# Optimization experiments

Measured on AMD Instinct MI355X. Metric: run time of the kernel, lower is better.

## Reference

```python
import jax, jax.numpy as jnp
import numpy as np


def _dilate(x, ker):
    """Grayscale (max-plus) dilation, TF tf.nn.dilation2d semantics, SAME pad, stride 1.

    x:   [B,H,W,C] or [B,H,W,C,F]
    ker: [kh,kw,C,F]
    out: [B,H,W,C,F] = max_{dy,dx} x_pad[b, h+dy, w+dx, c(,f)] + ker[dy,dx,c,f]
    """
    kh, kw = ker.shape[0], ker.shape[1]
    pt, pl = (kh - 1) // 2, (kw - 1) // 2
    pb, pr = kh - 1 - pt, kw - 1 - pl
    if x.ndim == 4:
        x = x[..., None]  # broadcast over filter axis
    B, H, W = x.shape[0], x.shape[1], x.shape[2]
    xp = jnp.pad(x, ((0, 0), (pt, pb), (pl, pr), (0, 0), (0, 0)),
                 constant_values=-jnp.inf)
    out = None
    for dy in range(kh):
        for dx in range(kw):
            v = xp[:, dy:dy + H, dx:dx + W] + ker[dy, dx]  # [B,H,W,C,F]
            out = v if out is None else jnp.maximum(out, v)
    return out


def _erode(x, ker):
    # TF identity: erosion2d(v, f) = -dilation2d(-v, spatially-flipped f)
    return -_dilate(-x, ker[::-1, ::-1])


def _opening_p4(x, kernel):
    # x: [B,4,H,W,C], kernel: [kh,kw,3,C,F]
    kero = jnp.stack([jnp.rot90(kernel[:, :, 2], 3, axes=(0, 1)),
                      kernel[:, :, 1],
                      jnp.rot90(kernel[:, :, 0], 1, axes=(0, 1))], axis=2)
    y = jnp.concatenate([x[:, -1:], x, x[:, :1]], axis=1)  # wrap group axis -> [B,6,H,W,C]
    ero = []
    for j in range(4):
        kr = jnp.rot90(kero, j, axes=(0, 1))  # [kh,kw,3,C,F]
        d = jnp.stack([_erode(y[:, j + k], kr[:, :, k]) for k in range(3)], axis=-1)
        ero.append(jnp.min(d, axis=-1))  # min over SE depth -> [B,H,W,C,F]
    ero = jnp.stack(ero, axis=1)  # [B,4,H,W,C,F]
    ep = jnp.concatenate([ero[:, -1:], ero, ero[:, :1]], axis=1)  # [B,6,H,W,C,F]
    outs = []
    for j in range(4):
        kr = jnp.rot90(kernel, j, axes=(0, 1))
        d = jnp.stack([_dilate(ep[:, j + k], kr[:, :, k]) for k in range(3)], axis=-1)
        outs.append(jnp.max(d, axis=-1))  # max over SE depth -> [B,H,W,C,F]
    open_res = jnp.stack(outs, axis=1)  # [B,4,H,W,C,F]
    return jnp.sum(open_res, axis=-2)   # sum over input channels -> [B,4,H,W,F]


def setup_inputs() -> dict:
    key = jax.random.key(0)
    k1, k2 = jax.random.split(key)
    x = jax.random.normal(k1, (4, 4, 64, 64, 8), dtype=jnp.float32)
    kernel = jax.random.normal(k2, (3, 3, 3, 8, 16), dtype=jnp.float32) * 0.1
    return {"x": x, "kernel": kernel}


def reference(x, kernel):
    return _opening_p4(x, kernel)
```

## Files before the change

kernel.cpp:

```cpp
#include <hip/hip_runtime.h>


#define HH 64
#define WW 64
#define NEG_INF (-__builtin_inff())
#define POS_INF (__builtin_inff())

#define ROT_G(G, A, B, I, J) do { switch (G) { \
    case 0:  I = (A);     J = (B);     break; \
    case 1:  I = (B);     J = 2 - (A); break; \
    case 2:  I = 2 - (A); J = 2 - (B); break; \
    default: I = 2 - (B); J = (A);     break; } } while (0)

typedef _Float16 hv4 __attribute__((ext_vector_type(4)));

__device__ __forceinline__ hv4 f4_to_hv4(float4 v) {
    hv4 r;
    r.x = (_Float16)v.x; r.y = (_Float16)v.y;
    r.z = (_Float16)v.z; r.w = (_Float16)v.w;
    return r;
}

__global__ __launch_bounds__(256) void erode_t(const float* __restrict__ x,
                                               const float* __restrict__ ker,
                                               hv4* __restrict__ ero) {
    __shared__ __align__(16) float xs[9 * 8 * 68];

    const int tid = threadIdx.x;
    const int h = blockIdx.x & 63;
    const int g = (blockIdx.x >> 6) & 3;
    const int b = blockIdx.x >> 8;

    const float4* x4 = (const float4*)x;
    const float4* ker4 = (const float4*)ker;

    for (int t = tid; t < 1188; t += 256) {
        int q01 = t & 1;
        int u = t >> 1;
        int wp = u % 66;
        int v = u / 66;
        int r = v % 3;
        int p = v / 3;
        int g2 = (g + p + 3) & 3;
        int h2 = h - 1 + r;
        int w2 = wp - 1;
        float4 vv;
        if ((unsigned)h2 < HH && (unsigned)w2 < WW)
            vv = x4[(((b * 4 + g2) * HH + h2) * WW + w2) * 2 + q01];
        else
            vv = make_float4(POS_INF, POS_INF, POS_INF, POS_INF);
        int rowb = (p * 3 + r) * 8 + q01 * 4;
        xs[(rowb + 0) * 68 + wp] = vv.x;
        xs[(rowb + 1) * 68 + wp] = vv.y;
        xs[(rowb + 2) * 68 + wp] = vv.z;
        xs[(rowb + 3) * 68 + wp] = vv.w;
    }
    __syncthreads();

    const int q = tid & 3;
    const int c = (tid >> 2) & 7;
    const int slot = tid >> 5;
    const float4* xs4 = (const float4*)xs;

    float4 acc[8];
#pragma unroll
    for (int i = 0; i < 8; ++i)
        acc[i] = make_float4(POS_INF, POS_INF, POS_INF, POS_INF);

#pragma unroll
    for (int k2 = 0; k2 < 3; ++k2) {
        float4 ke9[9];
#pragma unroll
        for (int t9 = 0; t9 < 9; ++t9) {
            int dy = t9 / 3, dx = t9 % 3;
            int a0 = 2 - dy, b0 = 2 - dx;
            int i, jj;
            ROT_G(g, a0, b0, i, jj);
            int ka, kb, kc;
            if (k2 == 0)      { ka = 2 - jj; kb = i;      kc = 2; }
            else if (k2 == 1) { ka = i;      kb = jj;     kc = 1; }
            else              { ka = jj;     kb = 2 - i;  kc = 0; }
            ke9[t9] = ker4[((ka * 3 + kb) * 3 + kc) * 32 + c * 4 + q];
        }
#pragma unroll
        for (int dy = 0; dy < 3; ++dy) {
            const int base4 = ((k2 * 3 + dy) * 8 + c) * 17 + slot * 2;
            float4 xa = xs4[base4];
            float4 xb = xs4[base4 + 1];
            float4 xc = xs4[base4 + 2];
            float xw[12] = {xa.x, xa.y, xa.z, xa.w,
                            xb.x, xb.y, xb.z, xb.w,
                            xc.x, xc.y, xc.z, xc.w};
#pragma unroll
            for (int dx = 0; dx < 3; ++dx) {
                float4 kv = ke9[dy * 3 + dx];
#pragma unroll
                for (int i = 0; i < 8; ++i) {
                    float v = xw[i + dx];
                    acc[i].x = fminf(acc[i].x, v - kv.x);
                    acc[i].y = fminf(acc[i].y, v - kv.y);
                    acc[i].z = fminf(acc[i].z, v - kv.z);
                    acc[i].w = fminf(acc[i].w, v - kv.w);
                }
            }
        }
    }

    const int row = (b * 4 + g) * HH + h;
    const size_t obase = ((size_t)row * 66 + slot * 8 + 1) * 32 + c * 4 + q;
#pragma unroll
    for (int i = 0; i < 8; ++i)
        ero[obase + (size_t)i * 32] = f4_to_hv4(acc[i]);

    const hv4 ninf = {(_Float16)NEG_INF, (_Float16)NEG_INF,
                      (_Float16)NEG_INF, (_Float16)NEG_INF};
    if (tid < 32)
        ero[(size_t)row * 66 * 32 + tid] = ninf;
    else if (tid < 64)
        ero[((size_t)row * 66 + 65) * 32 + (tid - 32)] = ninf;
}

__global__ __launch_bounds__(256) void dilate_t(const hv4* __restrict__ ero,
                                                const float* __restrict__ ker,
                                                float* __restrict__ out) {
    const int tid = threadIdx.x;
    const int q = tid & 3;
    const int c = (tid >> 2) & 7;
    const int slot = tid >> 5;
    const int ws = blockIdx.x & 7;
    const int hs = (blockIdx.x >> 3) & 7;
    const int j = (blockIdx.x >> 6) & 3;
    const int b = blockIdx.x >> 8;
    const int w = ws * 8 + slot;

    const float4* ker4 = (const float4*)ker;

    const hv4 ninf = {(_Float16)NEG_INF, (_Float16)NEG_INF,
                      (_Float16)NEG_INF, (_Float16)NEG_INF};
    hv4 acc[8];
#pragma unroll
    for (int r = 0; r < 8; ++r)
        acc[r] = ninf;

#pragma unroll
    for (int k = 0; k < 3; ++k) {
        const int gsrc = (j + k + 3) & 3;
        hv4 kd9[9];
#pragma unroll
        for (int t9 = 0; t9 < 9; ++t9) {
            int dy = t9 / 3, dx = t9 % 3;
            int i, jj;
            ROT_G(j, dy, dx, i, jj);
            kd9[t9] = f4_to_hv4(ker4[((i * 3 + jj) * 3 + k) * 32 + c * 4 + q]);
        }
        const size_t pb = ((size_t)(b * 4 + gsrc) * HH * 66 + w) * 32 + c * 4 + q;
#pragma unroll
        for (int ei = 0; ei < 10; ++ei) {
            const int er = hs * 8 - 1 + ei;
            if ((unsigned)er >= HH) continue;
            const size_t rb = pb + (size_t)er * 66 * 32;
            hv4 e0 = ero[rb];
            hv4 e1 = ero[rb + 32];
            hv4 e2 = ero[rb + 64];
#pragma unroll
            for (int dy = 0; dy < 3; ++dy) {
                const int rr = ei - dy;
                if ((unsigned)rr >= 8) continue;
                acc[rr] = __builtin_elementwise_max(acc[rr], e0 + kd9[dy * 3 + 0]);
                acc[rr] = __builtin_elementwise_max(acc[rr], e1 + kd9[dy * 3 + 1]);
                acc[rr] = __builtin_elementwise_max(acc[rr], e2 + kd9[dy * 3 + 2]);
            }
        }
    }

    float4* out4 = (float4*)out;
    const int bjbase = (b * 4 + j) * HH + hs * 8;
#pragma unroll
    for (int r = 0; r < 8; ++r) {
        float4 s = make_float4((float)acc[r].x, (float)acc[r].y,
                               (float)acc[r].z, (float)acc[r].w);
#pragma unroll
        for (int off = 4; off <= 16; off <<= 1) {
            s.x += __shfl_xor(s.x, off, 64);
            s.y += __shfl_xor(s.y, off, 64);
            s.z += __shfl_xor(s.z, off, 64);
            s.w += __shfl_xor(s.w, off, 64);
        }
        if (c == 0)
            out4[((size_t)(bjbase + r) * WW + w) * 4 + q] = s;
    }
}

__global__ __launch_bounds__(256, 3) void opening_fused_fb(
    const float* __restrict__ x, const float* __restrict__ ker, float* __restrict__ out)
{
    __shared__ __align__(16) float xs[8 * 4 * 144];
    __shared__ float4 es4[4 * 4 * 100];
    __shared__ float4 ke4[27 * 4 * 4];
    __shared__ float4 kd4[9 * 4 * 4];

    const int tid = threadIdx.x;
    const int tileX = blockIdx.x & 7;
    const int tileY = (blockIdx.x >> 3) & 7;
    const int j = (blockIdx.x >> 6) & 3;
    const int b = blockIdx.x >> 8;
    const float4* ker4 = (const float4*)ker;
    const float4* x4 = (const float4*)x;

    for (int t = tid; t < 1152; t += 256) {
        int q01 = t & 1;
        int cell = t >> 1;
        int g = cell / 144;
        int rem = cell - g * 144;
        int r = rem / 12;
        int s = rem - r * 12;
        int h = tileY * 8 - 2 + r;
        int w = tileX * 8 - 2 + s;
        float4 v;
        if ((unsigned)h < HH && (unsigned)w < WW)
            v = x4[(((b * 4 + g) * HH + h) * WW + w) * 2 + q01];
        else
            v = make_float4(POS_INF, POS_INF, POS_INF, POS_INF);
        int c0 = q01 * 4;
        xs[((c0 + 0) * 4 + g) * 144 + rem] = v.x;
        xs[((c0 + 1) * 4 + g) * 144 + rem] = v.y;
        xs[((c0 + 2) * 4 + g) * 144 + rem] = v.z;
        xs[((c0 + 3) * 4 + g) * 144 + rem] = v.w;
    }
    __syncthreads();

    const int q_o = tid & 3;
    const int ox = (tid >> 2) & 7;
    const int oy = tid >> 5;

    float4 acc[8];
#pragma unroll
    for (int c = 0; c < 8; ++c)
        acc[c] = make_float4(NEG_INF, NEG_INF, NEG_INF, NEG_INF);

    for (int k = 0; k < 3; ++k) {
        const int gsrc = (j + k + 3) & 3;
#pragma unroll
        for (int cg = 0; cg < 2; ++cg) {
            for (int t = tid; t < 576; t += 256) {
                if (t < 432) {
                    int q = t & 3;
                    int c4 = (t >> 2) & 3;
                    int tap = t >> 4;
                    int k2 = tap % 3;
                    int dxdy = tap / 3;
                    int dx = dxdy % 3;
                    int dy = dxdy / 3;
                    int a0 = 2 - dy, b0 = 2 - dx;
                    int i, jj;
                    ROT_G(gsrc, a0, b0, i, jj);
                    int ka, kb, kc;
                    if (k2 == 0)      { ka = 2 - jj; kb = i;      kc = 2; }
                    else if (k2 == 1) { ka = i;      kb = jj;     kc = 1; }
                    else              { ka = jj;     kb = 2 - i;  kc = 0; }
                    int c = cg * 4 + c4;
                    ke4[t] = ker4[((ka * 3 + kb) * 3 + kc) * 32 + c * 4 + q];
                } else {
                    int u = t - 432;
                    int q = u & 3;
                    int c4 = (u >> 2) & 3;
                    int dydx = u >> 4;
                    int dx = dydx % 3;
                    int dy = dydx / 3;
                    int i, jj;
                    ROT_G(j, dy, dx, i, jj);
                    int c = cg * 4 + c4;
                    kd4[u] = ker4[((i * 3 + jj) * 3 + k) * 32 + c * 4 + q];
                }
            }
            __syncthreads();

            for (int it = 0; it < 2; ++it) {
                int id = tid + (it << 8);
                int c4 = id >> 7;
                int p = id & 127;
                if (p >= 100) continue;
                int ey = (p * 205) >> 11;
                int ex = p - ey * 10;
                int h_es = tileY * 8 - 1 + ey;
                int w_es = tileX * 8 - 1 + ex;
                float4 b0, b1, b2, b3;
                if ((unsigned)h_es < HH && (unsigned)w_es < WW) {
                    b0 = b1 = b2 = b3 = make_float4(POS_INF, POS_INF, POS_INF, POS_INF);
                    int c = cg * 4 + c4;
#pragma unroll
                    for (int k2 = 0; k2 < 3; ++k2) {
                        int g2 = (gsrc + k2 + 3) & 3;
                        int base = (c * 4 + g2) * 144 + ey * 12 + ex;
#pragma unroll
                        for (int dy = 0; dy < 3; ++dy)
#pragma unroll
                            for (int dx = 0; dx < 3; ++dx) {
                                float v = xs[base + dy * 12 + dx];
                                const float4* kk = &ke4[(((dy * 3 + dx) * 3 + k2) * 4 + c4) * 4];
                                float4 kv;
                                kv = kk[0];
                                b0.x = fminf(b0.x, v - kv.x); b0.y = fminf(b0.y, v - kv.y);
                                b0.z = fminf(b0.z, v - kv.z); b0.w = fminf(b0.w, v - kv.w);
                                kv = kk[1];
                                b1.x = fminf(b1.x, v - kv.x); b1.y = fminf(b1.y, v - kv.y);
                                b1.z = fminf(b1.z, v - kv.z); b1.w = fminf(b1.w, v - kv.w);
                                kv = kk[2];
                                b2.x = fminf(b2.x, v - kv.x); b2.y = fminf(b2.y, v - kv.y);
                                b2.z = fminf(b2.z, v - kv.z); b2.w = fminf(b2.w, v - kv.w);
                                kv = kk[3];
                                b3.x = fminf(b3.x, v - kv.x); b3.y = fminf(b3.y, v - kv.y);
                                b3.z = fminf(b3.z, v - kv.z); b3.w = fminf(b3.w, v - kv.w);
                            }
                    }
                } else {
                    b0 = b1 = b2 = b3 = make_float4(NEG_INF, NEG_INF, NEG_INF, NEG_INF);
                }
                int eb = (c4 * 4) * 100 + p;
                es4[eb] = b0; es4[eb + 100] = b1; es4[eb + 200] = b2; es4[eb + 300] = b3;
            }
            __syncthreads();

#pragma unroll
            for (int c4 = 0; c4 < 4; ++c4) {
                float4 a = acc[cg * 4 + c4];
#pragma unroll
                for (int dy = 0; dy < 3; ++dy)
#pragma unroll
                    for (int dx = 0; dx < 3; ++dx) {
                        int pos = (oy + dy) * 10 + (ox + dx);
                        float4 e = es4[(c4 * 4 + q_o) * 100 + pos];
                        float4 kv = kd4[(dy * 3 + dx) * 16 + c4 * 4 + q_o];
                        a.x = fmaxf(a.x, e.x + kv.x);
                        a.y = fmaxf(a.y, e.y + kv.y);
                        a.z = fmaxf(a.z, e.z + kv.z);
                        a.w = fmaxf(a.w, e.w + kv.w);
                    }
                acc[cg * 4 + c4] = a;
            }
            __syncthreads();
        }
    }

    float4 s = acc[0];
#pragma unroll
    for (int c = 1; c < 8; ++c) {
        s.x += acc[c].x; s.y += acc[c].y; s.z += acc[c].z; s.w += acc[c].w;
    }
    const int h = tileY * 8 + oy;
    const int w = tileX * 8 + ox;
    ((float4*)out)[(((b * 4 + j) * HH + h) * WW + w) * 4 + q_o] = s;
}

extern "C" void kernel_launch(void* const* d_in, const int* in_sizes, int n_in,
                              void* d_out, int out_size, void* d_ws, size_t ws_size,
                              hipStream_t stream) {
    const float* x = (const float*)d_in[0];
    const float* ker = (const float*)d_in[1];
    float* out = (float*)d_out;

    const size_t ero_f16_bytes = (size_t)16 * HH * 66 * 32 * 8;

    if (ws_size >= ero_f16_bytes) {
        hv4* ero = (hv4*)d_ws;
        erode_t<<<1024, 256, 0, stream>>>(x, ker, ero);
        dilate_t<<<1024, 256, 0, stream>>>(ero, ker, out);
    } else {
        opening_fused_fb<<<1024, 256, 0, stream>>>(x, ker, out);
    }
}
```

Before: 91.31 us.

## Stage erosion tile in shared memory and compute all four rotations per block

The dilation kernel now loads a 4-group by 6-row by 10-column fp16 erosion halo tile into LDS once per block, then computes all four output rotations j from that shared tile, instead of each block re-reading global erosion data for a single j. Rows per block drop from 8 to 4 and the grid halves to 512 blocks. This removes redundant global loads, since each erosion group feeds three rotations. In exchange it adds LDS usage, a sync, more accumulator registers (16 hv4), a larger row-halo fraction and fewer blocks.

```diff
diff --git a/kernel.cpp b/kernel.cpp
--- a/kernel.cpp
+++ b/kernel.cpp
@@ -120,74 +120,103 @@
         ero[((size_t)row * 66 + 65) * 32 + (tid - 32)] = ninf;
 }
 
-__global__ __launch_bounds__(256) void dilate_t(const hv4* __restrict__ ero,
-                                                const float* __restrict__ ker,
-                                                float* __restrict__ out) {
+__global__ __launch_bounds__(256) void dilate_t2(const hv4* __restrict__ ero,
+                                                 const float* __restrict__ ker,
+                                                 float* __restrict__ out) {
+    __shared__ __align__(16) hv4 es[4 * 6 * 10 * 32];
+
     const int tid = threadIdx.x;
+    const int ws = blockIdx.x & 7;
+    const int hs = (blockIdx.x >> 3) & 15;
+    const int b = blockIdx.x >> 7;
+
+    {
+        const float4* ero4 = (const float4*)ero;
+        float4* es4 = (float4*)es;
+        const float nf = __uint_as_float(0xFC00FC00u);
+        const float4 ninf4 = make_float4(nf, nf, nf, nf);
+        for (int t = tid; t < 3840; t += 256) {
+            const int cq2 = t & 15;
+            const int rest = t >> 4;
+            const int wp10 = rest % 10;
+            const int ge = rest / 10;
+            const int ei = ge % 6;
+            const int gsrc = ge / 6;
+            const int er = hs * 4 - 1 + ei;
+            float4 v = ninf4;
+            if ((unsigned)er < HH)
+                v = ero4[(((b * 4 + gsrc) * HH + er) * 66 + ws * 8 + wp10) * 16 + cq2];
+            es4[rest * 16 + cq2] = v;
+        }
+    }
+    __syncthreads();
+
     const int q = tid & 3;
     const int c = (tid >> 2) & 7;
+    const int cq = tid & 31;
     const int slot = tid >> 5;
-    const int ws = blockIdx.x & 7;
-    const int hs = (blockIdx.x >> 3) & 7;
-    const int j = (blockIdx.x >> 6) & 3;
-    const int b = blockIdx.x >> 8;
-    const int w = ws * 8 + slot;
-
     const float4* ker4 = (const float4*)ker;
 
     const hv4 ninf = {(_Float16)NEG_INF, (_Float16)NEG_INF,
                       (_Float16)NEG_INF, (_Float16)NEG_INF};
-    hv4 acc[8];
-#pragma unroll
-    for (int r = 0; r < 8; ++r)
-        acc[r] = ninf;
-
-#pragma unroll
-    for (int k = 0; k < 3; ++k) {
-        const int gsrc = (j + k + 3) & 3;
-        hv4 kd9[9];
-#pragma unroll
-        for (int t9 = 0; t9 < 9; ++t9) {
-            int dy = t9 / 3, dx = t9 % 3;
-            int i, jj;
-            ROT_G(j, dy, dx, i, jj);
-            kd9[t9] = f4_to_hv4(ker4[((i * 3 + jj) * 3 + k) * 32 + c * 4 + q]);
-        }
-        const size_t pb = ((size_t)(b * 4 + gsrc) * HH * 66 + w) * 32 + c * 4 + q;
-#pragma unroll
-        for (int ei = 0; ei < 10; ++ei) {
-            const int er = hs * 8 - 1 + ei;
-            if ((unsigned)er >= HH) continue;
-            const size_t rb = pb + (size_t)er * 66 * 32;
-            hv4 e0 = ero[rb];
-            hv4 e1 = ero[rb + 32];
-            hv4 e2 = ero[rb + 64];
-#pragma unroll
-            for (int dy = 0; dy < 3; ++dy) {
-                const int rr = ei - dy;
-                if ((unsigned)rr >= 8) continue;
-                acc[rr] = __builtin_elementwise_max(acc[rr], e0 + kd9[dy * 3 + 0]);
-                acc[rr] = __builtin_elementwise_max(acc[rr], e1 + kd9[dy * 3 + 1]);
-                acc[rr] = __builtin_elementwise_max(acc[rr], e2 + kd9[dy * 3 + 2]);
+    hv4 acc[4][4];
+#pragma unroll
+    for (int j = 0; j < 4; ++j)
+#pragma unroll
+        for (int r = 0; r < 4; ++r)
+            acc[j][r] = ninf;
+
+#pragma unroll
+    for (int j = 0; j < 4; ++j) {
+#pragma unroll
+        for (int k = 0; k < 3; ++k) {
+            const int gsrc = (j + k + 3) & 3;
+            hv4 kd9[9];
+#pragma unroll
+            for (int t9 = 0; t9 < 9; ++t9) {
+                int dy = t9 / 3, dx = t9 % 3;
+                int i, jj;
+                ROT_G(j, dy, dx, i, jj);
+                kd9[t9] = f4_to_hv4(ker4[((i * 3 + jj) * 3 + k) * 32 + cq]);
+            }
+            const int pbase = gsrc * 1920 + slot * 32 + cq;
+#pragma unroll
+            for (int ei = 0; ei < 6; ++ei) {
+                const int rb = pbase + ei * 320;
+                hv4 e0 = es[rb];
+                hv4 e1 = es[rb + 32];
+                hv4 e2 = es[rb + 64];
+#pragma unroll
+                for (int dy = 0; dy < 3; ++dy) {
+                    const int rr = ei - dy;
+                    if (rr < 0 || rr >= 4) continue;
+                    acc[j][rr] = __builtin_elementwise_max(acc[j][rr], e0 + kd9[dy * 3 + 0]);
+                    acc[j][rr] = __builtin_elementwise_max(acc[j][rr], e1 + kd9[dy * 3 + 1]);
+                    acc[j][rr] = __builtin_elementwise_max(acc[j][rr], e2 + kd9[dy * 3 + 2]);
+                }
             }
         }
     }
 
     float4* out4 = (float4*)out;
-    const int bjbase = (b * 4 + j) * HH + hs * 8;
-#pragma unroll
-    for (int r = 0; r < 8; ++r) {
-        float4 s = make_float4((float)acc[r].x, (float)acc[r].y,
-                               (float)acc[r].z, (float)acc[r].w);
-#pragma unroll
-        for (int off = 4; off <= 16; off <<= 1) {
-            s.x += __shfl_xor(s.x, off, 64);
-            s.y += __shfl_xor(s.y, off, 64);
-            s.z += __shfl_xor(s.z, off, 64);
-            s.w += __shfl_xor(s.w, off, 64);
-        }
-        if (c == 0)
-            out4[((size_t)(bjbase + r) * WW + w) * 4 + q] = s;
+    const int w = ws * 8 + slot;
+#pragma unroll
+    for (int j = 0; j < 4; ++j) {
+        const int rowb = (b * 4 + j) * HH + hs * 4;
+#pragma unroll
+        for (int rr = 0; rr < 4; ++rr) {
+            float4 s = make_float4((float)acc[j][rr].x, (float)acc[j][rr].y,
+                                   (float)acc[j][rr].z, (float)acc[j][rr].w);
+#pragma unroll
+            for (int off = 4; off <= 16; off <<= 1) {
+                s.x += __shfl_xor(s.x, off, 64);
+                s.y += __shfl_xor(s.y, off, 64);
+                s.z += __shfl_xor(s.z, off, 64);
+                s.w += __shfl_xor(s.w, off, 64);
+            }
+            if (c == 0)
+                out4[((size_t)(rowb + rr) * WW + w) * 4 + q] = s;
+        }
     }
 }
 
@@ -364,7 +393,7 @@
     if (ws_size >= ero_f16_bytes) {
         hv4* ero = (hv4*)d_ws;
         erode_t<<<1024, 256, 0, stream>>>(x, ker, ero);
-        dilate_t<<<1024, 256, 0, stream>>>(ero, ker, out);
+        dilate_t2<<<512, 256, 0, stream>>>(ero, ker, out);
     } else {
         opening_fused_fb<<<1024, 256, 0, stream>>>(x, ker, out);
     }
```

Result: no change. 92.10 us (+0.9%).
